# Kernel tuning notes

Hardware: AMD Instinct MI355X
Metric: run time of the kernel (lower is better)

## Reference

```python
import jax, jax.numpy as jnp
import numpy as np

B, CHUNK = 8, 16
IMG = CHUNK * CHUNK   # 256; einsum patch-embed forces img_size = chunk_size**2
D = CHUNK * CHUNK     # d_model = chunk^2 = 256
H = D                 # pos-emb broadcast forces num_heads = chunk^2 = 256
DH = 1                # d_head = d_model // num_heads = 1
S = H + 1             # seq len after class token = 257
MLP = 1024
NCLS = 1000


def setup_inputs() -> dict:
    key = jax.random.key(0)
    ks = jax.random.split(key, 16)
    f = lambda k, sh: jax.random.normal(k, sh, dtype=jnp.float32) * 0.02
    return {
        'x': jax.random.normal(ks[0], (B, 1, IMG, IMG), dtype=jnp.float32),
        'class_token': f(ks[1], (1, 1, D)),
        'pos_emb': f(ks[2], (1, S, D)),
        'patch_w': jax.random.uniform(ks[3], (H, D, D), dtype=jnp.float32),  # torch.rand init
        'patch_b': jax.random.uniform(ks[4], (H, D), dtype=jnp.float32),
        'wq': f(ks[5], (H, D, DH)),
        'wk': f(ks[6], (H, D, DH)),
        'wv': f(ks[7], (H, D, DH)),
        'proj_w': f(ks[8], (D, D)),
        'proj_b': jnp.zeros((D,), jnp.float32),
        'mlp_w1': f(ks[9], (D, MLP)),
        'mlp_b1': jnp.zeros((MLP,), jnp.float32),
        'mlp_w2': f(ks[10], (MLP, D)),
        'mlp_b2': jnp.zeros((D,), jnp.float32),
        'ln1_g': jnp.ones((D,), jnp.float32),
        'ln1_b': jnp.zeros((D,), jnp.float32),
        'ln2_g': jnp.ones((D,), jnp.float32),
        'ln2_b': jnp.zeros((D,), jnp.float32),
        'head_w': f(ks[11], (D, NCLS)),
        'head_b': jnp.zeros((NCLS,), jnp.float32),
    }


def _ln(x, g, b, eps=1e-5):
    mu = x.mean(-1, keepdims=True)
    var = ((x - mu) ** 2).mean(-1, keepdims=True)
    return (x - mu) * jax.lax.rsqrt(var + eps) * g + b


def reference(x, class_token, pos_emb, patch_w, patch_b, wq, wk, wv, proj_w, proj_b,
              mlp_w1, mlp_b1, mlp_w2, mlp_b2, ln1_g, ln1_b, ln2_g, ln2_b, head_w, head_b):
    Bsz = x.shape[0]
    n = IMG // CHUNK  # patches per side = 16
    # crop: [B,1,img,img] -> [B, num_patches, chunk^2]
    p = x.reshape(Bsz, 1, n, CHUNK, n, CHUNK).transpose(0, 2, 4, 1, 3, 5).reshape(Bsz, n * n, CHUNK * CHUNK)
    # quirky per-position patch embed: [B, H, num_patches]
    t = jnp.einsum('bni,hni->bhn', p, patch_w) + patch_b[None]
    t = t.reshape(Bsz, -1, D)  # identity reshape here: [B, H, D] since num_patches == d_model
    cls = jnp.broadcast_to(class_token, (Bsz, 1, D))
    t = jnp.concatenate([cls, t], axis=1) + pos_emb  # [B, S, D]

    xn = _ln(t, ln1_g, ln1_b)  # same LN output used for q, k, v
    Q = jnp.einsum('bsd,hde->bhse', xn, wq)  # [B,H,S,1]
    K = jnp.einsum('bsd,hde->bhse', xn, wk)
    V = jnp.einsum('bsd,hde->bhse', xn, wv)
    scores = jnp.einsum('bhse,bhte->bhst', Q, K) / jnp.sqrt(jnp.float32(DH))
    attn = jax.nn.softmax(scores, axis=-1)  # [B,H,S,S]
    o = jnp.einsum('bhst,bhte->bhse', attn, V)  # [B,H,S,1]
    o = o.transpose(0, 2, 1, 3).reshape(Bsz, S, H * DH)  # concat heads -> [B,S,D]
    t = t + o @ proj_w + proj_b

    xn2 = _ln(t, ln2_g, ln2_b)
    h = jax.nn.gelu(xn2 @ mlp_w1 + mlp_b1, approximate=False)
    t = t + h @ mlp_w2 + mlp_b2

    logits = t[:, 0] @ head_w + head_b
    return jax.nn.softmax(logits, axis=-1)
```

## Files before the change

### kernel.cpp

```cpp
#include <hip/hip_runtime.h>
#include <math.h>

#define Bsz   8
#define D     256
#define S     257
#define MLP   1024
#define NCLS  1000
#define M_ROWS (Bsz * S)

typedef unsigned int u32;
typedef unsigned short u16;
typedef __attribute__((ext_vector_type(8))) short bshort8;
typedef __attribute__((ext_vector_type(4))) float f32x4;

__device__ __forceinline__ float wave_sum(float v) {
  #pragma unroll
  for (int m = 1; m < 64; m <<= 1) v += __shfl_xor(v, m, 64);
  return v;
}

__device__ __forceinline__ u16 f2bf(float f) {
  u32 u = __float_as_uint(f);
  u += 0x7FFFu + ((u >> 16) & 1u);
  return (u16)(u >> 16);
}
__device__ __forceinline__ float bf2f(u16 h) { return __uint_as_float(((u32)h) << 16); }
__device__ __forceinline__ u32 pk2(u16 a, u16 b) { return (u32)a | ((u32)b << 16); }
__device__ __forceinline__ float fexp2(float x) { return __builtin_amdgcn_exp2f(x); }

__device__ __forceinline__ void patch_body(int blk, int tid,
                                           const float* __restrict__ x,
                                           const float* __restrict__ pw,
                                           const float* __restrict__ pb,
                                           const float* __restrict__ pos,
                                           const float* __restrict__ ct,
                                           float* __restrict__ t,
                                           char* smem) {
  u16* sAh = (u16*)smem;
  u16* sAl = (u16*)(smem + 8192);
  u16* sBh = (u16*)(smem + 16384);
  u16* sBl = (u16*)(smem + 24576);
  const int n = blk >> 2;
  const int col0 = (blk & 3) * 64;
  const int pi = n >> 4, pj = n & 15;
  const int lane = tid & 63;
  const int w = tid >> 6;
  const int fr = lane & 15, g = lane >> 4;
  const int sr = tid >> 2, sc = tid & 3;
  const int arow = sr > 7 ? 7 : sr;
  const u32 off0 = (u32)(sr * 128) + ((u32)((2 * sc)     ^ (sr & 7)) << 4);
  const u32 off1 = (u32)(sr * 128) + ((u32)((2 * sc + 1) ^ (sr & 7)) << 4);
  const float* ap32 = x + (size_t)arow * 65536 + (size_t)(pi * 16) * 256 + pj * 16;
  const float* bp32 = pw + (size_t)(col0 + sr) * 65536 + (size_t)n * 256 + sc * 16;

  if ((blk & 3) == 0 && tid < 8)
    t[((size_t)tid * S) * D + n] = ct[n] + pos[n];

  f32x4 acc = {0, 0, 0, 0}, ac2 = {0, 0, 0, 0};

  for (int k0 = 0; k0 < 256; k0 += 64) {
    const float* asrc = ap32 + (size_t)((k0 >> 4) + sc) * 256;
    float fa[16], fb[16];
    #pragma unroll
    for (int i = 0; i < 4; ++i) {
      float4 f4 = *(const float4*)(asrc + i * 4);
      fa[i*4+0] = f4.x; fa[i*4+1] = f4.y; fa[i*4+2] = f4.z; fa[i*4+3] = f4.w;
      float4 g4 = *(const float4*)(bp32 + k0 + i * 4);
      fb[i*4+0] = g4.x; fb[i*4+1] = g4.y; fb[i*4+2] = g4.z; fb[i*4+3] = g4.w;
    }
    u16 ah16[16], al16[16], bh16[16], bl16[16];
    #pragma unroll
    for (int i = 0; i < 16; ++i) {
      u16 h = f2bf(fa[i]); ah16[i] = h; al16[i] = f2bf(fa[i] - bf2f(h));
      u16 hb = f2bf(fb[i]); bh16[i] = hb; bl16[i] = f2bf(fb[i] - bf2f(hb));
    }
    __syncthreads();
    *(uint4*)((char*)sAh + off0) = make_uint4(pk2(ah16[0],ah16[1]), pk2(ah16[2],ah16[3]), pk2(ah16[4],ah16[5]), pk2(ah16[6],ah16[7]));
    *(uint4*)((char*)sAh + off1) = make_uint4(pk2(ah16[8],ah16[9]), pk2(ah16[10],ah16[11]), pk2(ah16[12],ah16[13]), pk2(ah16[14],ah16[15]));
    *(uint4*)((char*)sAl + off0) = make_uint4(pk2(al16[0],al16[1]), pk2(al16[2],al16[3]), pk2(al16[4],al16[5]), pk2(al16[6],al16[7]));
    *(uint4*)((char*)sAl + off1) = make_uint4(pk2(al16[8],al16[9]), pk2(al16[10],al16[11]), pk2(al16[12],al16[13]), pk2(al16[14],al16[15]));
    *(uint4*)((char*)sBh + off0) = make_uint4(pk2(bh16[0],bh16[1]), pk2(bh16[2],bh16[3]), pk2(bh16[4],bh16[5]), pk2(bh16[6],bh16[7]));
    *(uint4*)((char*)sBh + off1) = make_uint4(pk2(bh16[8],bh16[9]), pk2(bh16[10],bh16[11]), pk2(bh16[12],bh16[13]), pk2(bh16[14],bh16[15]));
    *(uint4*)((char*)sBl + off0) = make_uint4(pk2(bl16[0],bl16[1]), pk2(bl16[2],bl16[3]), pk2(bl16[4],bl16[5]), pk2(bl16[6],bl16[7]));
    *(uint4*)((char*)sBl + off1) = make_uint4(pk2(bl16[8],bl16[9]), pk2(bl16[10],bl16[11]), pk2(bl16[12],bl16[13]), pk2(bl16[14],bl16[15]));
    __syncthreads();
    #pragma unroll
    for (int ks = 0; ks < 2; ++ks) {
      int rA = fr;
      u32 oa = (u32)(rA * 128) + ((u32)((ks * 4 + g) ^ (rA & 7)) << 4);
      bshort8 ah = *(const bshort8*)((const char*)sAh + oa);
      bshort8 al = *(const bshort8*)((const char*)sAl + oa);
      int rB = w * 16 + fr;
      u32 ob = (u32)(rB * 128) + ((u32)((ks * 4 + g) ^ (rB & 7)) << 4);
      bshort8 bh = *(const bshort8*)((const char*)sBh + ob);
      bshort8 bl = *(const bshort8*)((const char*)sBl + ob);
      acc = __builtin_amdgcn_mfma_f32_16x16x32_bf16(ah, bh, acc, 0, 0, 0);
      ac2 = __builtin_amdgcn_mfma_f32_16x16x32_bf16(ah, bl, ac2, 0, 0, 0);
      ac2 = __builtin_amdgcn_mfma_f32_16x16x32_bf16(al, bh, ac2, 0, 0, 0);
    }
  }
  if (g < 2) {
    int h = col0 + w * 16 + fr;
    float addend = pb[h * 256 + n] + pos[(1 + h) * 256 + n];
    #pragma unroll
    for (int r = 0; r < 4; ++r) {
      int b = g * 4 + r;
      t[((size_t)b * S + 1 + h) * D + n] = acc[r] + ac2[r] + addend;
    }
  }
}

__device__ __forceinline__ void conv_copy2_body(int blk, int tid,
                                                const float* __restrict__ wk,
                                                const float* __restrict__ wv,
                                                u16* __restrict__ W) {
  int wsel = blk >> 6, tile = blk & 63;
  const float* src = wsel == 0 ? wk : wv;
  u16* oh = W + wsel * 131072;
  u16* ol = oh + 65536;
  int r0 = (tile >> 3) * 32, c0 = (tile & 7) * 32;
  int tr = tid >> 3, tc = (tid & 7) * 4;
  const float4 f = *(const float4*)(src + (size_t)(r0 + tr) * 256 + c0 + tc);
  u16 h0 = f2bf(f.x), h1 = f2bf(f.y), h2 = f2bf(f.z), h3 = f2bf(f.w);
  u16 l0 = f2bf(f.x - bf2f(h0)), l1 = f2bf(f.y - bf2f(h1));
  u16 l2 = f2bf(f.z - bf2f(h2)), l3 = f2bf(f.w - bf2f(h3));
  size_t o = (size_t)(r0 + tr) * 256 + c0 + tc;
  *(uint2*)(oh + o) = make_uint2(pk2(h0, h1), pk2(h2, h3));
  *(uint2*)(ol + o) = make_uint2(pk2(l0, l1), pk2(l2, l3));
}

__device__ __forceinline__ void prefetch_body(int blk, int tid,
                                              const float* __restrict__ p, int nfloat) {
  int base = blk * 4096 + tid * 4;
  float acc = 0.f;
  #pragma unroll
  for (int i = 0; i < 4; ++i) {
    int idx = base + i * 1024;
    if (idx + 3 < nfloat) {
      float4 f = *(const float4*)(p + idx);
      acc += (f.x + f.y) + (f.z + f.w);
    }
  }
  asm volatile("" :: "v"(acc));
}

__global__ __launch_bounds__(256) void stage0(const float* __restrict__ x,
                                              const float* __restrict__ pw,
                                              const float* __restrict__ pb,
                                              const float* __restrict__ pos,
                                              const float* __restrict__ ct,
                                              const float* __restrict__ wk,
                                              const float* __restrict__ wv,
                                              const float* __restrict__ proj_w,
                                              const float* __restrict__ mlp_w1,
                                              const float* __restrict__ mlp_w2,
                                              const float* __restrict__ head_w,
                                              u16* __restrict__ Wkv,
                                              float* __restrict__ t) {
  __shared__ __align__(16) char smem[32768];
  int blk = blockIdx.x, tid = threadIdx.x;
  if (blk < 1024)      patch_body(blk, tid, x, pw, pb, pos, ct, t, smem);
  else if (blk < 1152) conv_copy2_body(blk - 1024, tid, wk, wv, Wkv);
  else {
    int p = blk - 1152;
    if (p < 16)       prefetch_body(p, tid, proj_w, 65536);
    else if (p < 80)  prefetch_body(p - 16, tid, mlp_w1, 262144);
    else if (p < 144) prefetch_body(p - 80, tid, mlp_w2, 262144);
    else              prefetch_body(p - 144, tid, head_w, 256000);
  }
}

__global__ __launch_bounds__(256) void ln_split(const float* __restrict__ in,
                                                u16* __restrict__ oh,
                                                u16* __restrict__ ol,
                                                const float* __restrict__ g,
                                                const float* __restrict__ b,
                                                int nrows) {
  int wid = threadIdx.x >> 6, lane = threadIdx.x & 63;
  int row = blockIdx.x * 4 + wid;
  if (row >= nrows) return;
  const float* p = in + (size_t)row * D;
  float4 v = *(const float4*)&p[lane * 4];
  float s = wave_sum(v.x + v.y + v.z + v.w);
  float mu = s * (1.0f / 256.0f);
  float dx = v.x - mu, dy = v.y - mu, dz = v.z - mu, dw = v.w - mu;
  float q = wave_sum(dx * dx + dy * dy + dz * dz + dw * dw);
  float rs = 1.0f / sqrtf(q * (1.0f / 256.0f) + 1e-5f);
  float4 gv = *(const float4*)&g[lane * 4];
  float4 bv = *(const float4*)&b[lane * 4];
  float o0 = dx * rs * gv.x + bv.x;
  float o1 = dy * rs * gv.y + bv.y;
  float o2 = dz * rs * gv.z + bv.z;
  float o3 = dw * rs * gv.w + bv.w;
  u16 h0 = f2bf(o0), h1 = f2bf(o1), h2 = f2bf(o2), h3 = f2bf(o3);
  u16 l0 = f2bf(o0 - bf2f(h0)), l1 = f2bf(o1 - bf2f(h1));
  u16 l2 = f2bf(o2 - bf2f(h2)), l3 = f2bf(o3 - bf2f(h3));
  size_t o = (size_t)row * D + lane * 4;
  *(uint2*)(oh + o) = make_uint2(pk2(h0, h1), pk2(h2, h3));
  *(uint2*)(ol + o) = make_uint2(pk2(l0, l1), pk2(l2, l3));
}

template<int OUTT>
__device__ __forceinline__ void gemm_core(const u16* __restrict__ A16,
                                          const u16* __restrict__ A16l,
                                          const u16* __restrict__ Bh,
                                          const u16* __restrict__ Bl,
                                          float* __restrict__ Cf,
                                          int M, int N, int K, int row0, int col0) {
  __shared__ __align__(16) u16 sAh[4096];
  __shared__ __align__(16) u16 sAl[4096];
  __shared__ __align__(16) u16 sBh[4096];
  __shared__ __align__(16) u16 sBl[4096];
  const int tid = threadIdx.x;
  const int lane = tid & 63;
  const int w = tid >> 6, wm = w >> 1, wn = w & 1;
  const int fr = lane & 15, g = lane >> 4;
  const int sr = tid >> 2, sc = tid & 3;
  int arow = row0 + sr; if (arow > M - 1) arow = M - 1;
  const u32 off0 = (u32)(sr * 128) + ((u32)((2 * sc)     ^ (sr & 7)) << 4);
  const u32 off1 = (u32)(sr * 128) + ((u32)((2 * sc + 1) ^ (sr & 7)) << 4);
  const u16* ap16  = A16  + (size_t)arow * K + sc * 16;
  const u16* ap16l = A16l + (size_t)arow * K + sc * 16;
  const u16* bhp = Bh + (size_t)(col0 + sr) * K + sc * 16;
  const u16* blp = Bl + (size_t)(col0 + sr) * K + sc * 16;

  f32x4 acc[2][2], ac2[2][2];
  #pragma unroll
  for (int i = 0; i < 2; ++i)
    #pragma unroll
    for (int j = 0; j < 2; ++j) { acc[i][j] = (f32x4){0,0,0,0}; ac2[i][j] = (f32x4){0,0,0,0}; }

  for (int k0 = 0; k0 < K; k0 += 64) {
    uint4 wAh0 = *(const uint4*)(ap16 + k0);
    uint4 wAh1 = *(const uint4*)(ap16 + k0 + 8);
    uint4 wAl0 = *(const uint4*)(ap16l + k0);
    uint4 wAl1 = *(const uint4*)(ap16l + k0 + 8);
    uint4 wBh0 = *(const uint4*)(bhp + k0);
    uint4 wBh1 = *(const uint4*)(bhp + k0 + 8);
    uint4 wBl0 = *(const uint4*)(blp + k0);
    uint4 wBl1 = *(const uint4*)(blp + k0 + 8);
    __syncthreads();
    *(uint4*)((char*)sAh + off0) = wAh0;
    *(uint4*)((char*)sAh + off1) = wAh1;
    *(uint4*)((char*)sAl + off0) = wAl0;
    *(uint4*)((char*)sAl + off1) = wAl1;
    *(uint4*)((char*)sBh + off0) = wBh0;
    *(uint4*)((char*)sBh + off1) = wBh1;
    *(uint4*)((char*)sBl + off0) = wBl0;
    *(uint4*)((char*)sBl + off1) = wBl1;
    __syncthreads();
    #pragma unroll
    for (int ks = 0; ks < 2; ++ks) {
      bshort8 ah[2], al[2], bh2[2], bl2[2];
      #pragma unroll
      for (int f = 0; f < 2; ++f) {
        int rA = wm * 32 + f * 16 + fr;
        u32 oa = (u32)(rA * 128) + ((u32)((ks * 4 + g) ^ (rA & 7)) << 4);
        ah[f] = *(const bshort8*)((const char*)sAh + oa);
        al[f] = *(const bshort8*)((const char*)sAl + oa);
        int rB = wn * 32 + f * 16 + fr;
        u32 ob = (u32)(rB * 128) + ((u32)((ks * 4 + g) ^ (rB & 7)) << 4);
        bh2[f] = *(const bshort8*)((const char*)sBh + ob);
        bl2[f] = *(const bshort8*)((const char*)sBl + ob);
      }
      #pragma unroll
      for (int fi = 0; fi < 2; ++fi)
        #pragma unroll
        for (int fj = 0; fj < 2; ++fj) {
          acc[fi][fj] = __builtin_amdgcn_mfma_f32_16x16x32_bf16(ah[fi], bh2[fj], acc[fi][fj], 0, 0, 0);
          ac2[fi][fj] = __builtin_amdgcn_mfma_f32_16x16x32_bf16(ah[fi], bl2[fj], ac2[fi][fj], 0, 0, 0);
          ac2[fi][fj] = __builtin_amdgcn_mfma_f32_16x16x32_bf16(al[fi], bh2[fj], ac2[fi][fj], 0, 0, 0);
        }
    }
  }
  #pragma unroll
  for (int fi = 0; fi < 2; ++fi) {
    #pragma unroll
    for (int fj = 0; fj < 2; ++fj) {
      int col = col0 + wn * 32 + fj * 16 + fr;
      int rbase = row0 + wm * 32 + fi * 16 + g * 4;
      #pragma unroll
      for (int r = 0; r < 4; ++r) {
        int row = rbase + r;
        if (row < M) {
          float v = acc[fi][fj][r] + ac2[fi][fj][r];
          if (OUTT) {
            u32 bq = (u32)row / 257u;
            u32 sq = (u32)row - bq * 257u;
            Cf[((size_t)bq * 256 + col) * 257 + sq] = v;
          } else {
            Cf[(size_t)row * N + col] = v;
          }
        }
      }
    }
  }
}

__global__ __launch_bounds__(256) void kv_kernel(const u16* __restrict__ xnh,
                                                 const u16* __restrict__ xnl,
                                                 const u16* __restrict__ Wkv,
                                                 float* __restrict__ kk,
                                                 float* __restrict__ v) {
  int z = blockIdx.z;
  const u16* Bh = Wkv + z * 131072;
  const u16* Bl = Bh + 65536;
  float* C = z == 0 ? kk : v;
  gemm_core<1>(xnh, xnl, Bh, Bl, C, M_ROWS, 256, 256, blockIdx.y * 64, blockIdx.x * 64);
}

__global__ __launch_bounds__(256) void attn_cls(const u16* __restrict__ xnh,
                                                const u16* __restrict__ xnl,
                                                const float* __restrict__ wq,
                                                const float* __restrict__ Kb,
                                                const float* __restrict__ Vb,
                                                float* __restrict__ o_cls) {
  __shared__ float red[20];
  int h = blockIdx.x, b = blockIdx.y;
  int tid = threadIdx.x, wid = tid >> 6, lane = tid & 63;
  size_t xbase = (size_t)b * 257 * 256;
  float xv = bf2f(xnh[xbase + tid]) + bf2f(xnl[xbase + tid]);
  float part = xv * wq[h * 256 + tid];
  part = wave_sum(part);
  size_t rowbase = ((size_t)b * 256 + h) * 257;
  float kt = Kb[rowbase + tid], vt = Vb[rowbase + tid];
  float k2 = 0.f, v2 = 0.f;
  if (tid == 0) { k2 = Kb[rowbase + 256]; v2 = Vb[rowbase + 256]; }
  float lmax = tid == 0 ? fmaxf(kt, k2) : kt;
  float lmin = tid == 0 ? fminf(kt, k2) : kt;
  #pragma unroll
  for (int m = 1; m < 64; m <<= 1) {
    lmax = fmaxf(lmax, __shfl_xor(lmax, m, 64));
    lmin = fminf(lmin, __shfl_xor(lmin, m, 64));
  }
  if (lane == 0) { red[wid] = part; red[4 + wid] = lmax; red[8 + wid] = lmin; }
  __syncthreads();
  float q = (red[0] + red[1]) + (red[2] + red[3]);
  float kmax = fmaxf(fmaxf(red[4], red[5]), fmaxf(red[6], red[7]));
  float kmin = fminf(fminf(red[8], red[9]), fminf(red[10], red[11]));
  const float L2E = 1.4426950408889634f;
  float m = q >= 0.f ? q * kmax : q * kmin;
  float ql = q * L2E, nml = -m * L2E;
  float e = fexp2(fmaf(ql, kt, nml));
  float den = e, num = e * vt;
  if (tid == 0) {
    float e2 = fexp2(fmaf(ql, k2, nml));
    den += e2; num = fmaf(e2, v2, num);
  }
  den = wave_sum(den); num = wave_sum(num);
  if (lane == 0) { red[12 + wid] = den; red[16 + wid] = num; }
  __syncthreads();
  if (tid == 0) {
    float dd = (red[12] + red[13]) + (red[14] + red[15]);
    float nn = (red[16] + red[17]) + (red[18] + red[19]);
    o_cls[b * 256 + h] = nn / dd;
  }
}


__global__ __launch_bounds__(256) void proj_part(const float* __restrict__ o_cls,
                                                 const float* __restrict__ proj_w,
                                                 float* __restrict__ pA) {
  int b = blockIdx.x >> 3, kq = blockIdx.x & 7;
  int n = threadIdx.x;
  const float* ob = o_cls + b * 256 + kq * 32;
  const float* wp = proj_w + (size_t)(kq * 32) * 256 + n;
  float a0 = 0.f, a1 = 0.f, a2 = 0.f, a3 = 0.f;
  #pragma unroll
  for (int k = 0; k < 32; k += 4) {
    a0 = fmaf(ob[k + 0], wp[(size_t)(k + 0) * 256], a0);
    a1 = fmaf(ob[k + 1], wp[(size_t)(k + 1) * 256], a1);
    a2 = fmaf(ob[k + 2], wp[(size_t)(k + 2) * 256], a2);
    a3 = fmaf(ob[k + 3], wp[(size_t)(k + 3) * 256], a3);
  }
  pA[((size_t)kq * 8 + b) * 256 + n] = (a0 + a1) + (a2 + a3);
}

__global__ __launch_bounds__(256) void proj_red_ln(const float* __restrict__ pA,
                                                   const float* __restrict__ proj_b,
                                                   const float* __restrict__ t,
                                                   const float* __restrict__ ln2_g,
                                                   const float* __restrict__ ln2_b,
                                                   float* __restrict__ tnbuf,
                                                   float* __restrict__ xn2) {
  __shared__ float red[8];
  int b = blockIdx.x, n = threadIdx.x;
  int wid = n >> 6, lane = n & 63;
  float s = t[((size_t)b * S) * D + n] + proj_b[n];
  #pragma unroll
  for (int kq = 0; kq < 8; ++kq) s += pA[((size_t)kq * 8 + b) * 256 + n];
  tnbuf[b * 256 + n] = s;
  float s1 = wave_sum(s);
  if (lane == 0) red[wid] = s1;
  __syncthreads();
  float mu = ((red[0] + red[1]) + (red[2] + red[3])) * (1.0f / 256.0f);
  float dx = s - mu;
  float s2 = wave_sum(dx * dx);
  if (lane == 0) red[4 + wid] = s2;
  __syncthreads();
  float var = ((red[4] + red[5]) + (red[6] + red[7])) * (1.0f / 256.0f);
  float rs = 1.0f / sqrtf(var + 1e-5f);
  xn2[b * 256 + n] = dx * rs * ln2_g[n] + ln2_b[n];
}

__global__ __launch_bounds__(256) void mlp1_part(const float* __restrict__ xn2,
                                                 const float* __restrict__ mlp_w1,
                                                 float* __restrict__ pB) {
  __shared__ float xs[8][32];
  int nc = blockIdx.x >> 3, kq = blockIdx.x & 7;
  int tid = threadIdx.x;
  {
    int b = tid >> 5, kk = tid & 31;
    xs[b][kk] = xn2[b * 256 + kq * 32 + kk];
  }
  __syncthreads();
  int n = nc * 256 + tid;
  const float* wp = mlp_w1 + (size_t)(kq * 32) * 1024 + n;
  float acc[8] = {0, 0, 0, 0, 0, 0, 0, 0};
  #pragma unroll
  for (int k = 0; k < 32; ++k) {
    float w = wp[(size_t)k * 1024];
    #pragma unroll
    for (int b = 0; b < 8; ++b) acc[b] = fmaf(xs[b][k], w, acc[b]);
  }
  #pragma unroll
  for (int b = 0; b < 8; ++b) pB[((size_t)kq * 8 + b) * 1024 + n] = acc[b];
}

__global__ __launch_bounds__(256) void mlp1_red(const float* __restrict__ pB,
                                                const float* __restrict__ mlp_b1,
                                                float* __restrict__ hrow) {
  int elem = blockIdx.x * 256 + threadIdx.x;
  int b = elem >> 10, n = elem & 1023;
  float s = mlp_b1[n];
  #pragma unroll
  for (int kq = 0; kq < 8; ++kq) s += pB[((size_t)kq * 8 + b) * 1024 + n];
  hrow[b * 1024 + n] = 0.5f * s * (1.0f + erff(s * 0.70710678118654752440f));
}

__global__ __launch_bounds__(256) void mlp2_part(const float* __restrict__ hrow,
                                                 const float* __restrict__ mlp_w2,
                                                 float* __restrict__ pC) {
  __shared__ float hs[8][32];
  int kq = blockIdx.x;
  int tid = threadIdx.x;
  {
    int b = tid >> 5, kk = tid & 31;
    hs[b][kk] = hrow[b * 1024 + kq * 32 + kk];
  }
  __syncthreads();
  int n = tid;
  const float* wp = mlp_w2 + (size_t)(kq * 32) * 256 + n;
  float acc[8] = {0, 0, 0, 0, 0, 0, 0, 0};
  #pragma unroll
  for (int k = 0; k < 32; ++k) {
    float w = wp[(size_t)k * 256];
    #pragma unroll
    for (int b = 0; b < 8; ++b) acc[b] = fmaf(hs[b][k], w, acc[b]);
  }
  #pragma unroll
  for (int b = 0; b < 8; ++b) pC[((size_t)kq * 8 + b) * 256 + n] = acc[b];
}

__global__ __launch_bounds__(256) void mlp2_red(const float* __restrict__ pC,
                                                const float* __restrict__ mlp_b2,
                                                const float* __restrict__ tnbuf,
                                                float* __restrict__ tn2) {
  int b = blockIdx.x, n = threadIdx.x;
  float s = tnbuf[b * 256 + n] + mlp_b2[n];
  #pragma unroll
  for (int kq = 0; kq < 32; ++kq) s += pC[((size_t)kq * 8 + b) * 256 + n];
  tn2[b * 256 + n] = s;
}

__global__ __launch_bounds__(256) void head_part(const float* __restrict__ tn2,
                                                 const float* __restrict__ head_w,
                                                 float* __restrict__ pD) {
  __shared__ float ts[8][32];
  int nc = blockIdx.x >> 3, kq = blockIdx.x & 7;
  int tid = threadIdx.x;
  {
    int b = tid >> 5, kk = tid & 31;
    ts[b][kk] = tn2[b * 256 + kq * 32 + kk];
  }
  __syncthreads();
  int nn = tid & 127, dq = tid >> 7;
  int n = nc * 128 + nn;
  bool valid = n < NCLS;
  const float* wp = head_w + (size_t)(kq * 32 + dq * 16) * NCLS + n;
  float acc[8] = {0, 0, 0, 0, 0, 0, 0, 0};
  #pragma unroll
  for (int k = 0; k < 16; ++k) {
    float w = valid ? wp[(size_t)k * NCLS] : 0.f;
    int kk = dq * 16 + k;
    #pragma unroll
    for (int b = 0; b < 8; ++b) acc[b] = fmaf(ts[b][kk], w, acc[b]);
  }
  #pragma unroll
  for (int b = 0; b < 8; ++b)
    pD[(((size_t)(kq * 2 + dq)) * 8 + b) * 1024 + n] = acc[b];
}

__global__ __launch_bounds__(256) void softmax_kernel(const float* __restrict__ pD,
                                                      const float* __restrict__ head_b,
                                                      float* __restrict__ out) {
  __shared__ float red[8];
  int b = blockIdx.x, tid = threadIdx.x;
  int wid = tid >> 6, lane = tid & 63;
  float v[4];
  #pragma unroll
  for (int i = 0; i < 4; ++i) {
    int n = i * 256 + tid;
    if (n < NCLS) {
      float s = head_b[n];
      #pragma unroll
      for (int q = 0; q < 16; ++q) s += pD[((size_t)q * 8 + b) * 1024 + n];
      v[i] = s;
    } else {
      v[i] = -1e30f;
    }
  }
  float mx = fmaxf(fmaxf(v[0], v[1]), fmaxf(v[2], v[3]));
  #pragma unroll
  for (int s = 1; s < 64; s <<= 1) mx = fmaxf(mx, __shfl_xor(mx, s, 64));
  if (lane == 0) red[wid] = mx;
  __syncthreads();
  float gmax = fmaxf(fmaxf(red[0], red[1]), fmaxf(red[2], red[3]));
  float e[4], ssum = 0.f;
  #pragma unroll
  for (int i = 0; i < 4; ++i) {
    e[i] = expf(v[i] - gmax);
    if (i * 256 + tid >= NCLS) e[i] = 0.f;
    ssum += e[i];
  }
  ssum = wave_sum(ssum);
  if (lane == 0) red[4 + wid] = ssum;
  __syncthreads();
  float inv = 1.0f / ((red[4] + red[5]) + (red[6] + red[7]));
  #pragma unroll
  for (int i = 0; i < 4; ++i) {
    int n = i * 256 + tid;
    if (n < NCLS) out[(size_t)b * NCLS + n] = e[i] * inv;
  }
}

extern "C" void kernel_launch(void* const* d_in, const int* in_sizes, int n_in,
                              void* d_out, int out_size, void* d_ws, size_t ws_size,
                              hipStream_t stream) {
  const float* x        = (const float*)d_in[0];
  const float* class_tk = (const float*)d_in[1];
  const float* pos_emb  = (const float*)d_in[2];
  const float* patch_w  = (const float*)d_in[3];
  const float* patch_b  = (const float*)d_in[4];
  const float* wq       = (const float*)d_in[5];
  const float* wk       = (const float*)d_in[6];
  const float* wv       = (const float*)d_in[7];
  const float* proj_w   = (const float*)d_in[8];
  const float* proj_b   = (const float*)d_in[9];
  const float* mlp_w1   = (const float*)d_in[10];
  const float* mlp_b1   = (const float*)d_in[11];
  const float* mlp_w2   = (const float*)d_in[12];
  const float* mlp_b2   = (const float*)d_in[13];
  const float* ln1_g    = (const float*)d_in[14];
  const float* ln1_b    = (const float*)d_in[15];
  const float* ln2_g    = (const float*)d_in[16];
  const float* ln2_b    = (const float*)d_in[17];
  const float* head_w   = (const float*)d_in[18];
  const float* head_b   = (const float*)d_in[19];
  float* out = (float*)d_out;

  float* ws = (float*)d_ws;
  const size_t NTOK = (size_t)M_ROWS * D;
  float* t     = ws;
  u16*  xnh    = (u16*)(ws + NTOK);
  u16*  xnl    = xnh + NTOK;
  float* kk    = ws + 2 * NTOK;
  float* v     = ws + 3 * NTOK;
  float* ocls  = ws + 4 * NTOK;
  u16*  Wkv    = (u16*)(ws + 4 * NTOK + 4096);
  float* TAIL  = ws + 5 * NTOK;
  float* tnbuf = TAIL;
  float* xn2   = TAIL + 2048;
  float* hrow  = TAIL + 4096;
  float* tn2   = TAIL + 12288;
  float* pA    = TAIL + 16384;
  float* pB    = pA + 16384;
  float* pC    = pB + 65536;
  float* pD    = pC + 65536;

  stage0<<<1359, 256, 0, stream>>>(x, patch_w, patch_b, pos_emb, class_tk,
                                   wk, wv, proj_w, mlp_w1, mlp_w2, head_w, Wkv, t);

  ln_split<<<(M_ROWS + 3) / 4, 256, 0, stream>>>(t, xnh, xnl, ln1_g, ln1_b, M_ROWS);

  kv_kernel<<<dim3(4, 33, 2), 256, 0, stream>>>(xnh, xnl, Wkv, kk, v);

  attn_cls<<<dim3(256, Bsz), 256, 0, stream>>>(xnh, xnl, wq, kk, v, ocls);

  proj_part<<<64, 256, 0, stream>>>(ocls, proj_w, pA);
  proj_red_ln<<<Bsz, 256, 0, stream>>>(pA, proj_b, t, ln2_g, ln2_b, tnbuf, xn2);

  mlp1_part<<<32, 256, 0, stream>>>(xn2, mlp_w1, pB);
  mlp1_red<<<32, 256, 0, stream>>>(pB, mlp_b1, hrow);

  mlp2_part<<<32, 256, 0, stream>>>(hrow, mlp_w2, pC);
  mlp2_red<<<Bsz, 256, 0, stream>>>(pC, mlp_b2, tnbuf, tn2);

  head_part<<<64, 256, 0, stream>>>(tn2, head_w, pD);
  softmax_kernel<<<Bsz, 256, 0, stream>>>(pD, head_b, out);
}
```

Baseline: 64.78 us.

## Fuse tail kernels into one persistent kernel with global atomic barriers

Replaces the eight small tail kernels (projection, LN2, MLP1, GELU, MLP2, head, softmax) with one 64-block kernel that separates phases with a software grid barrier built on an atomic counter. The counter is reset inside attn_cls. The MLP stages are repartitioned so all 64 blocks take part, which enlarges the partial-sum buffers. The aim is to remove per-launch overhead and gaps between tiny kernels. In exchange it relies on all 64 blocks being co-resident and pays for spin-wait barriers.

New measurement: 84.24 us. 30.0% more time.

```diff
diff --git a/kernel.cpp b/kernel.cpp
--- a/kernel.cpp
+++ b/kernel.cpp
@@ -7,6 +7,7 @@
 #define MLP   1024
 #define NCLS  1000
 #define M_ROWS (Bsz * S)
+#define TBLK  64
 
 typedef unsigned int u32;
 typedef unsigned short u16;
@@ -27,6 +28,18 @@
 __device__ __forceinline__ float bf2f(u16 h) { return __uint_as_float(((u32)h) << 16); }
 __device__ __forceinline__ u32 pk2(u16 a, u16 b) { return (u32)a | ((u32)b << 16); }
 __device__ __forceinline__ float fexp2(float x) { return __builtin_amdgcn_exp2f(x); }
+
+__device__ __forceinline__ void gbar(u32* cnt, int phase) {
+  __syncthreads();
+  if (threadIdx.x == 0) {
+    __threadfence();
+    atomicAdd(cnt, 1u);
+    u32 target = (u32)TBLK * (u32)(phase + 1);
+    while (atomicAdd(cnt, 0u) < target) __builtin_amdgcn_s_sleep(2);
+    __threadfence();
+  }
+  __syncthreads();
+}
 
 __device__ __forceinline__ void patch_body(int blk, int tid,
                                            const float* __restrict__ x,
@@ -314,10 +327,12 @@
                                                 const float* __restrict__ wq,
                                                 const float* __restrict__ Kb,
                                                 const float* __restrict__ Vb,
-                                                float* __restrict__ o_cls) {
+                                                float* __restrict__ o_cls,
+                                                u32* __restrict__ cnt) {
   __shared__ float red[20];
   int h = blockIdx.x, b = blockIdx.y;
   int tid = threadIdx.x, wid = tid >> 6, lane = tid & 63;
+  if (h == 0 && b == 0 && tid == 0) *cnt = 0u;
   size_t xbase = (size_t)b * 257 * 256;
   float xv = bf2f(xnh[xbase + tid]) + bf2f(xnl[xbase + tid]);
   float part = xv * wq[h * 256 + tid];
@@ -357,190 +372,194 @@
   }
 }
 
-
-__global__ __launch_bounds__(256) void proj_part(const float* __restrict__ o_cls,
-                                                 const float* __restrict__ proj_w,
-                                                 float* __restrict__ pA) {
-  int b = blockIdx.x >> 3, kq = blockIdx.x & 7;
-  int n = threadIdx.x;
-  const float* ob = o_cls + b * 256 + kq * 32;
-  const float* wp = proj_w + (size_t)(kq * 32) * 256 + n;
-  float a0 = 0.f, a1 = 0.f, a2 = 0.f, a3 = 0.f;
-  #pragma unroll
-  for (int k = 0; k < 32; k += 4) {
-    a0 = fmaf(ob[k + 0], wp[(size_t)(k + 0) * 256], a0);
-    a1 = fmaf(ob[k + 1], wp[(size_t)(k + 1) * 256], a1);
-    a2 = fmaf(ob[k + 2], wp[(size_t)(k + 2) * 256], a2);
-    a3 = fmaf(ob[k + 3], wp[(size_t)(k + 3) * 256], a3);
-  }
-  pA[((size_t)kq * 8 + b) * 256 + n] = (a0 + a1) + (a2 + a3);
-}
-
-__global__ __launch_bounds__(256) void proj_red_ln(const float* __restrict__ pA,
-                                                   const float* __restrict__ proj_b,
-                                                   const float* __restrict__ t,
-                                                   const float* __restrict__ ln2_g,
-                                                   const float* __restrict__ ln2_b,
-                                                   float* __restrict__ tnbuf,
-                                                   float* __restrict__ xn2) {
+__global__ __launch_bounds__(256) void tail_fused(const float* __restrict__ o_cls,
+                                                  const float* __restrict__ proj_w,
+                                                  const float* __restrict__ proj_b,
+                                                  const float* __restrict__ t,
+                                                  const float* __restrict__ ln2_g,
+                                                  const float* __restrict__ ln2_b,
+                                                  const float* __restrict__ mlp_w1,
+                                                  const float* __restrict__ mlp_b1,
+                                                  const float* __restrict__ mlp_w2,
+                                                  const float* __restrict__ mlp_b2,
+                                                  const float* __restrict__ head_w,
+                                                  const float* __restrict__ head_b,
+                                                  float* __restrict__ tnbuf,
+                                                  float* __restrict__ xn2,
+                                                  float* __restrict__ hrow,
+                                                  float* __restrict__ tn2,
+                                                  float* __restrict__ pA,
+                                                  float* __restrict__ pB,
+                                                  float* __restrict__ pC,
+                                                  float* __restrict__ pD,
+                                                  u32* __restrict__ cnt,
+                                                  float* __restrict__ out) {
+  __shared__ float smem[8][32];
   __shared__ float red[8];
-  int b = blockIdx.x, n = threadIdx.x;
-  int wid = n >> 6, lane = n & 63;
-  float s = t[((size_t)b * S) * D + n] + proj_b[n];
-  #pragma unroll
-  for (int kq = 0; kq < 8; ++kq) s += pA[((size_t)kq * 8 + b) * 256 + n];
-  tnbuf[b * 256 + n] = s;
-  float s1 = wave_sum(s);
-  if (lane == 0) red[wid] = s1;
-  __syncthreads();
-  float mu = ((red[0] + red[1]) + (red[2] + red[3])) * (1.0f / 256.0f);
-  float dx = s - mu;
-  float s2 = wave_sum(dx * dx);
-  if (lane == 0) red[4 + wid] = s2;
-  __syncthreads();
-  float var = ((red[4] + red[5]) + (red[6] + red[7])) * (1.0f / 256.0f);
-  float rs = 1.0f / sqrtf(var + 1e-5f);
-  xn2[b * 256 + n] = dx * rs * ln2_g[n] + ln2_b[n];
-}
-
-__global__ __launch_bounds__(256) void mlp1_part(const float* __restrict__ xn2,
-                                                 const float* __restrict__ mlp_w1,
-                                                 float* __restrict__ pB) {
-  __shared__ float xs[8][32];
-  int nc = blockIdx.x >> 3, kq = blockIdx.x & 7;
-  int tid = threadIdx.x;
+  const int blk = blockIdx.x, tid = threadIdx.x;
+  const int wid = tid >> 6, lane = tid & 63;
+
   {
-    int b = tid >> 5, kk = tid & 31;
-    xs[b][kk] = xn2[b * 256 + kq * 32 + kk];
-  }
-  __syncthreads();
-  int n = nc * 256 + tid;
-  const float* wp = mlp_w1 + (size_t)(kq * 32) * 1024 + n;
-  float acc[8] = {0, 0, 0, 0, 0, 0, 0, 0};
-  #pragma unroll
-  for (int k = 0; k < 32; ++k) {
-    float w = wp[(size_t)k * 1024];
-    #pragma unroll
-    for (int b = 0; b < 8; ++b) acc[b] = fmaf(xs[b][k], w, acc[b]);
-  }
-  #pragma unroll
-  for (int b = 0; b < 8; ++b) pB[((size_t)kq * 8 + b) * 1024 + n] = acc[b];
-}
-
-__global__ __launch_bounds__(256) void mlp1_red(const float* __restrict__ pB,
-                                                const float* __restrict__ mlp_b1,
-                                                float* __restrict__ hrow) {
-  int elem = blockIdx.x * 256 + threadIdx.x;
-  int b = elem >> 10, n = elem & 1023;
-  float s = mlp_b1[n];
-  #pragma unroll
-  for (int kq = 0; kq < 8; ++kq) s += pB[((size_t)kq * 8 + b) * 1024 + n];
-  hrow[b * 1024 + n] = 0.5f * s * (1.0f + erff(s * 0.70710678118654752440f));
-}
-
-__global__ __launch_bounds__(256) void mlp2_part(const float* __restrict__ hrow,
-                                                 const float* __restrict__ mlp_w2,
-                                                 float* __restrict__ pC) {
-  __shared__ float hs[8][32];
-  int kq = blockIdx.x;
-  int tid = threadIdx.x;
+    int b = blk >> 3, kq = blk & 7;
+    const float* ob = o_cls + b * 256 + kq * 32;
+    const float* wp = proj_w + (size_t)(kq * 32) * 256 + tid;
+    float a0 = 0.f, a1 = 0.f, a2 = 0.f, a3 = 0.f;
+    #pragma unroll
+    for (int k = 0; k < 32; k += 4) {
+      a0 = fmaf(ob[k + 0], wp[(size_t)(k + 0) * 256], a0);
+      a1 = fmaf(ob[k + 1], wp[(size_t)(k + 1) * 256], a1);
+      a2 = fmaf(ob[k + 2], wp[(size_t)(k + 2) * 256], a2);
+      a3 = fmaf(ob[k + 3], wp[(size_t)(k + 3) * 256], a3);
+    }
+    pA[((size_t)kq * 8 + b) * 256 + tid] = (a0 + a1) + (a2 + a3);
+  }
+  gbar(cnt, 0);
+
+  if (blk < 8) {
+    int b = blk, n = tid;
+    float s = t[((size_t)b * S) * D + n] + proj_b[n];
+    #pragma unroll
+    for (int kq = 0; kq < 8; ++kq) s += pA[((size_t)kq * 8 + b) * 256 + n];
+    tnbuf[b * 256 + n] = s;
+    float s1 = wave_sum(s);
+    if (lane == 0) red[wid] = s1;
+    __syncthreads();
+    float mu = ((red[0] + red[1]) + (red[2] + red[3])) * (1.0f / 256.0f);
+    float dx = s - mu;
+    float s2 = wave_sum(dx * dx);
+    if (lane == 0) red[4 + wid] = s2;
+    __syncthreads();
+    float var = ((red[4] + red[5]) + (red[6] + red[7])) * (1.0f / 256.0f);
+    float rs = 1.0f / sqrtf(var + 1e-5f);
+    xn2[b * 256 + n] = dx * rs * ln2_g[n] + ln2_b[n];
+  }
+  gbar(cnt, 1);
+
   {
-    int b = tid >> 5, kk = tid & 31;
-    hs[b][kk] = hrow[b * 1024 + kq * 32 + kk];
-  }
-  __syncthreads();
-  int n = tid;
-  const float* wp = mlp_w2 + (size_t)(kq * 32) * 256 + n;
-  float acc[8] = {0, 0, 0, 0, 0, 0, 0, 0};
-  #pragma unroll
-  for (int k = 0; k < 32; ++k) {
-    float w = wp[(size_t)k * 256];
-    #pragma unroll
-    for (int b = 0; b < 8; ++b) acc[b] = fmaf(hs[b][k], w, acc[b]);
-  }
-  #pragma unroll
-  for (int b = 0; b < 8; ++b) pC[((size_t)kq * 8 + b) * 256 + n] = acc[b];
-}
-
-__global__ __launch_bounds__(256) void mlp2_red(const float* __restrict__ pC,
-                                                const float* __restrict__ mlp_b2,
-                                                const float* __restrict__ tnbuf,
-                                                float* __restrict__ tn2) {
-  int b = blockIdx.x, n = threadIdx.x;
-  float s = tnbuf[b * 256 + n] + mlp_b2[n];
-  #pragma unroll
-  for (int kq = 0; kq < 32; ++kq) s += pC[((size_t)kq * 8 + b) * 256 + n];
-  tn2[b * 256 + n] = s;
-}
-
-__global__ __launch_bounds__(256) void head_part(const float* __restrict__ tn2,
-                                                 const float* __restrict__ head_w,
-                                                 float* __restrict__ pD) {
-  __shared__ float ts[8][32];
-  int nc = blockIdx.x >> 3, kq = blockIdx.x & 7;
-  int tid = threadIdx.x;
+    int nc = blk >> 4, kq = blk & 15;
+    if (tid < 128) {
+      int b = tid >> 4, kk = tid & 15;
+      smem[b][kk] = xn2[b * 256 + kq * 16 + kk];
+    }
+    __syncthreads();
+    int n = nc * 256 + tid;
+    const float* wp = mlp_w1 + (size_t)(kq * 16) * 1024 + n;
+    float acc[8] = {0, 0, 0, 0, 0, 0, 0, 0};
+    #pragma unroll
+    for (int k = 0; k < 16; ++k) {
+      float w = wp[(size_t)k * 1024];
+      #pragma unroll
+      for (int b = 0; b < 8; ++b) acc[b] = fmaf(smem[b][k], w, acc[b]);
+    }
+    #pragma unroll
+    for (int b = 0; b < 8; ++b) pB[((size_t)kq * 8 + b) * 1024 + n] = acc[b];
+  }
+  gbar(cnt, 2);
+
+  if (blk < 32) {
+    int elem = blk * 256 + tid;
+    int b = elem >> 10, n = elem & 1023;
+    float s = mlp_b1[n];
+    #pragma unroll
+    for (int kq = 0; kq < 16; ++kq) s += pB[((size_t)kq * 8 + b) * 1024 + n];
+    hrow[b * 1024 + n] = 0.5f * s * (1.0f + erff(s * 0.70710678118654752440f));
+  }
+  gbar(cnt, 3);
+
   {
-    int b = tid >> 5, kk = tid & 31;
-    ts[b][kk] = tn2[b * 256 + kq * 32 + kk];
-  }
-  __syncthreads();
-  int nn = tid & 127, dq = tid >> 7;
-  int n = nc * 128 + nn;
-  bool valid = n < NCLS;
-  const float* wp = head_w + (size_t)(kq * 32 + dq * 16) * NCLS + n;
-  float acc[8] = {0, 0, 0, 0, 0, 0, 0, 0};
-  #pragma unroll
-  for (int k = 0; k < 16; ++k) {
-    float w = valid ? wp[(size_t)k * NCLS] : 0.f;
-    int kk = dq * 16 + k;
-    #pragma unroll
-    for (int b = 0; b < 8; ++b) acc[b] = fmaf(ts[b][kk], w, acc[b]);
-  }
-  #pragma unroll
-  for (int b = 0; b < 8; ++b)
-    pD[(((size_t)(kq * 2 + dq)) * 8 + b) * 1024 + n] = acc[b];
-}
-
-__global__ __launch_bounds__(256) void softmax_kernel(const float* __restrict__ pD,
-                                                      const float* __restrict__ head_b,
-                                                      float* __restrict__ out) {
-  __shared__ float red[8];
-  int b = blockIdx.x, tid = threadIdx.x;
-  int wid = tid >> 6, lane = tid & 63;
-  float v[4];
-  #pragma unroll
-  for (int i = 0; i < 4; ++i) {
-    int n = i * 256 + tid;
-    if (n < NCLS) {
-      float s = head_b[n];
+    int kq = blk;
+    __syncthreads();
+    if (tid < 128) {
+      int b = tid >> 4, kk = tid & 15;
+      smem[b][kk] = hrow[b * 1024 + kq * 16 + kk];
+    }
+    __syncthreads();
+    const float* wp = mlp_w2 + (size_t)(kq * 16) * 256 + tid;
+    float acc[8] = {0, 0, 0, 0, 0, 0, 0, 0};
+    #pragma unroll
+    for (int k = 0; k < 16; ++k) {
+      float w = wp[(size_t)k * 256];
       #pragma unroll
-      for (int q = 0; q < 16; ++q) s += pD[((size_t)q * 8 + b) * 1024 + n];
-      v[i] = s;
-    } else {
-      v[i] = -1e30f;
-    }
-  }
-  float mx = fmaxf(fmaxf(v[0], v[1]), fmaxf(v[2], v[3]));
-  #pragma unroll
-  for (int s = 1; s < 64; s <<= 1) mx = fmaxf(mx, __shfl_xor(mx, s, 64));
-  if (lane == 0) red[wid] = mx;
-  __syncthreads();
-  float gmax = fmaxf(fmaxf(red[0], red[1]), fmaxf(red[2], red[3]));
-  float e[4], ssum = 0.f;
-  #pragma unroll
-  for (int i = 0; i < 4; ++i) {
-    e[i] = expf(v[i] - gmax);
-    if (i * 256 + tid >= NCLS) e[i] = 0.f;
-    ssum += e[i];
-  }
-  ssum = wave_sum(ssum);
-  if (lane == 0) red[4 + wid] = ssum;
-  __syncthreads();
-  float inv = 1.0f / ((red[4] + red[5]) + (red[6] + red[7]));
-  #pragma unroll
-  for (int i = 0; i < 4; ++i) {
-    int n = i * 256 + tid;
-    if (n < NCLS) out[(size_t)b * NCLS + n] = e[i] * inv;
+      for (int b = 0; b < 8; ++b) acc[b] = fmaf(smem[b][k], w, acc[b]);
+    }
+    #pragma unroll
+    for (int b = 0; b < 8; ++b) pC[((size_t)kq * 8 + b) * 256 + tid] = acc[b];
+  }
+  gbar(cnt, 4);
+
+  if (blk < 8) {
+    int b = blk, n = tid;
+    float s = tnbuf[b * 256 + n] + mlp_b2[n];
+    #pragma unroll
+    for (int kq = 0; kq < 64; ++kq) s += pC[((size_t)kq * 8 + b) * 256 + n];
+    tn2[b * 256 + n] = s;
+  }
+  gbar(cnt, 5);
+
+  {
+    int nc = blk >> 3, kq = blk & 7;
+    __syncthreads();
+    {
+      int b = tid >> 5, kk = tid & 31;
+      smem[b][kk] = tn2[b * 256 + kq * 32 + kk];
+    }
+    __syncthreads();
+    int nn = tid & 127, dq = tid >> 7;
+    int n = nc * 128 + nn;
+    bool valid = n < NCLS;
+    const float* wp = head_w + (size_t)(kq * 32 + dq * 16) * NCLS + n;
+    float acc[8] = {0, 0, 0, 0, 0, 0, 0, 0};
+    #pragma unroll
+    for (int k = 0; k < 16; ++k) {
+      float w = valid ? wp[(size_t)k * NCLS] : 0.f;
+      int kk = dq * 16 + k;
+      #pragma unroll
+      for (int b = 0; b < 8; ++b) acc[b] = fmaf(smem[b][kk], w, acc[b]);
+    }
+    #pragma unroll
+    for (int b = 0; b < 8; ++b)
+      pD[(((size_t)(kq * 2 + dq)) * 8 + b) * 1024 + n] = acc[b];
+  }
+  gbar(cnt, 6);
+
+  if (blk < 8) {
+    int b = blk;
+    float v[4];
+    #pragma unroll
+    for (int i = 0; i < 4; ++i) {
+      int n = i * 256 + tid;
+      if (n < NCLS) {
+        float s = head_b[n];
+        #pragma unroll
+        for (int q = 0; q < 16; ++q) s += pD[((size_t)q * 8 + b) * 1024 + n];
+        v[i] = s;
+      } else {
+        v[i] = -1e30f;
+      }
+    }
+    float mx = fmaxf(fmaxf(v[0], v[1]), fmaxf(v[2], v[3]));
+    #pragma unroll
+    for (int s = 1; s < 64; s <<= 1) mx = fmaxf(mx, __shfl_xor(mx, s, 64));
+    __syncthreads();
+    if (lane == 0) red[wid] = mx;
+    __syncthreads();
+    float gmax = fmaxf(fmaxf(red[0], red[1]), fmaxf(red[2], red[3]));
+    float e[4], ssum = 0.f;
+    #pragma unroll
+    for (int i = 0; i < 4; ++i) {
+      e[i] = expf(v[i] - gmax);
+      if (i * 256 + tid >= NCLS) e[i] = 0.f;
+      ssum += e[i];
+    }
+    ssum = wave_sum(ssum);
+    if (lane == 0) red[4 + wid] = ssum;
+    __syncthreads();
+    float inv = 1.0f / ((red[4] + red[5]) + (red[6] + red[7]));
+    #pragma unroll
+    for (int i = 0; i < 4; ++i) {
+      int n = i * 256 + tid;
+      if (n < NCLS) out[(size_t)b * NCLS + n] = e[i] * inv;
+    }
   }
 }
 
@@ -583,10 +602,11 @@
   float* xn2   = TAIL + 2048;
   float* hrow  = TAIL + 4096;
   float* tn2   = TAIL + 12288;
+  u32*   cnt   = (u32*)(TAIL + 14336);
   float* pA    = TAIL + 16384;
   float* pB    = pA + 16384;
-  float* pC    = pB + 65536;
-  float* pD    = pC + 65536;
+  float* pC    = pB + 131072;
+  float* pD    = pC + 131072;
 
   stage0<<<1359, 256, 0, stream>>>(x, patch_w, patch_b, pos_emb, class_tk,
                                    wk, wv, proj_w, mlp_w1, mlp_w2, head_w, Wkv, t);
@@ -595,17 +615,11 @@
 
   kv_kernel<<<dim3(4, 33, 2), 256, 0, stream>>>(xnh, xnl, Wkv, kk, v);
 
-  attn_cls<<<dim3(256, Bsz), 256, 0, stream>>>(xnh, xnl, wq, kk, v, ocls);
-
-  proj_part<<<64, 256, 0, stream>>>(ocls, proj_w, pA);
-  proj_red_ln<<<Bsz, 256, 0, stream>>>(pA, proj_b, t, ln2_g, ln2_b, tnbuf, xn2);
-
-  mlp1_part<<<32, 256, 0, stream>>>(xn2, mlp_w1, pB);
-  mlp1_red<<<32, 256, 0, stream>>>(pB, mlp_b1, hrow);
-
-  mlp2_part<<<32, 256, 0, stream>>>(hrow, mlp_w2, pC);
-  mlp2_red<<<Bsz, 256, 0, stream>>>(pC, mlp_b2, tnbuf, tn2);
-
-  head_part<<<64, 256, 0, stream>>>(tn2, head_w, pD);
-  softmax_kernel<<<Bsz, 256, 0, stream>>>(pD, head_b, out);
-}
+  attn_cls<<<dim3(256, Bsz), 256, 0, stream>>>(xnh, xnl, wq, kk, v, ocls, cnt);
+
+  tail_fused<<<TBLK, 256, 0, stream>>>(ocls, proj_w, proj_b, t, ln2_g, ln2_b,
+                                       mlp_w1, mlp_b1, mlp_w2, mlp_b2,
+                                       head_w, head_b,
+                                       tnbuf, xn2, hrow, tn2, pA, pB, pC, pD,
+                                       cnt, out);
+}
```
